# Performance work log

Measured on AMD Instinct MI355X. Metric: run time of the kernel, lower is better.

Reference implementation:

```python
import jax, jax.numpy as jnp
import numpy as np

# Phi-2 config
B, S = 4, 1024            # batch, seq_len (uniform prefill)
T = B * S                 # total tokens
HID = 2560
H = 32                    # attention heads
D = HID // H              # head_size = 80
ROT = int(0.4 * D)        # partial rotary dim = 32
THETA = 10000.0
SCALE = D ** -0.5
NUM_SLOTS = 2 * T


def setup_inputs() -> dict:
    key = jax.random.key(0)
    ks = jax.random.split(key, 6)
    hidden_states = jax.random.normal(ks[0], (T, HID), jnp.float32) * 0.02
    # true rope tables: positions restart per sequence
    pos = jnp.tile(jnp.arange(S, dtype=jnp.float32), B)                 # [T]
    inv_freq = 1.0 / (THETA ** (jnp.arange(0, ROT, 2, dtype=jnp.float32) / ROT))  # [ROT/2]
    freqs = pos[:, None] * inv_freq[None, :]                            # [T, ROT/2]
    cos, sin = jnp.cos(freqs), jnp.sin(freqs)
    slots = jnp.arange(T, dtype=jnp.int32)
    kv_cache_k = jnp.zeros((NUM_SLOTS, H, D), jnp.float32)
    kv_cache_v = jnp.zeros((NUM_SLOTS, H, D), jnp.float32)
    qkv_w = jax.random.normal(ks[1], (3 * HID, HID), jnp.float32) * 0.02
    qkv_b = jax.random.normal(ks[2], (3 * HID,), jnp.float32) * 0.02
    dense_w = jax.random.normal(ks[3], (HID, HID), jnp.float32) * 0.02
    dense_b = jax.random.normal(ks[4], (HID,), jnp.float32) * 0.02
    return {"hidden_states": hidden_states, "cos": cos, "sin": sin, "slots": slots,
            "kv_cache_k": kv_cache_k, "kv_cache_v": kv_cache_v,
            "qkv_w": qkv_w, "qkv_b": qkv_b, "dense_w": dense_w, "dense_b": dense_b}


def _partial_rope(x, cos, sin):
    # x: [T, H, D]; rotate-half rope on the first ROT dims only
    x1 = x[..., : ROT // 2]
    x2 = x[..., ROT // 2 : ROT]
    c = cos[:, None, :]  # [T,1,ROT/2]
    s = sin[:, None, :]
    rot = jnp.concatenate([x1 * c - x2 * s, x1 * s + x2 * c], axis=-1)
    return jnp.concatenate([rot, x[..., ROT:]], axis=-1)


def reference(hidden_states, cos, sin, slots, kv_cache_k, kv_cache_v,
              qkv_w, qkv_b, dense_w, dense_b):
    # fused QKV projection
    qkv = hidden_states @ qkv_w.T + qkv_b                 # [T, 3*HID]
    q = qkv[:, :HID].reshape(T, H, D)
    k = qkv[:, HID:2 * HID].reshape(T, H, D)
    v = qkv[:, 2 * HID:].reshape(T, H, D)
    # partial rotary on q and k
    q = _partial_rope(q, cos, sin)
    k = _partial_rope(k, cos, sin)
    # KV-cache write (reshape_and_cache)
    kc = kv_cache_k.at[slots].set(k)
    vc = kv_cache_v.at[slots].set(v)
    # causal flash-attention (prefill path), uniform seq lengths
    qb = q.reshape(B, S, H, D)
    kb = k.reshape(B, S, H, D)
    vb = v.reshape(B, S, H, D)
    scores = jnp.einsum("bqhd,bkhd->bhqk", qb, kb) * SCALE  # [B,H,S,S]
    causal = jnp.tril(jnp.ones((S, S), bool))
    scores = jnp.where(causal[None, None], scores, jnp.finfo(scores.dtype).min)
    probs = jax.nn.softmax(scores, axis=-1)
    attn = jnp.einsum("bhqk,bkhd->bqhd", probs, vb).reshape(T, HID)
    out = attn @ dense_w.T + dense_b                       # [T, HID]
    return out, kc, vc
```

## Files before the change

### kernel.cpp

```cpp
#include <hip/hip_runtime.h>

#define SEQ    1024
#define NBAT   4
#define TTOK   4096
#define HIDN   2560
#define NQKV   7680
#define NHEAD  32
#define DHEAD  80
#define NSLOT  8192
#define SCALE_F 0.111803398874989485f
#define LOG2E_F 1.4426950408889634f

typedef float  f32x4  __attribute__((ext_vector_type(4)));
typedef __bf16 bf16x8 __attribute__((ext_vector_type(8)));
typedef short  s16x8  __attribute__((ext_vector_type(8)));
typedef short  s16x4  __attribute__((ext_vector_type(4)));
typedef ushort u16x4  __attribute__((ext_vector_type(4)));

typedef __attribute__((address_space(3))) void lds_v;
typedef __attribute__((address_space(1))) void glb_v;

__device__ __forceinline__ void gload16(const void* g, void* l) {
  __builtin_amdgcn_global_load_lds((glb_v*)g, (lds_v*)l, 16, 0, 0);
}

__device__ __forceinline__ f32x4 mfma16(s16x8 a, s16x8 b, f32x4 c) {
  return __builtin_amdgcn_mfma_f32_16x16x32_bf16(
      __builtin_bit_cast(bf16x8, a), __builtin_bit_cast(bf16x8, b), c, 0, 0, 0);
}

__device__ __forceinline__ ushort f2bf(float f) {
  uint u = __builtin_bit_cast(uint, f);
  u += 0x7fffu + ((u >> 16) & 1u);
  return (ushort)(u >> 16);
}
__device__ __forceinline__ float bf2f(ushort h) {
  uint u = (uint)h << 16;
  return __builtin_bit_cast(float, u);
}

#define NQ_HS  2621440
#define NQ_QW  4915200
#define NQ_DW  1638400
#define NQ_PRE (NQ_HS + NQ_QW)
__global__ __launch_bounds__(256)
void prep_kernel(const float* __restrict__ hs, const float* __restrict__ qkvw,
                 ushort* __restrict__ hsb, ushort* __restrict__ qkvwb,
                 uint* __restrict__ flags) {
  const int tid0 = blockIdx.x * 256 + threadIdx.x;
  if (tid0 < NSLOT) flags[tid0] = 0u;
  const int stride = gridDim.x * 256;
  for (int i = tid0; i < NQ_PRE; i += stride) {
    const float* src; ushort* dst; int q;
    if (i < NQ_HS) { src = hs;   dst = hsb;   q = i; }
    else           { src = qkvw; dst = qkvwb; q = i - NQ_HS; }
    float4 v = *(const float4*)(src + q * 4);
    u16x4 o = { f2bf(v.x), f2bf(v.y), f2bf(v.z), f2bf(v.w) };
    *(u16x4*)(dst + q * 4) = o;
  }
}

template<int OUT_BF16>
__global__ __launch_bounds__(512, 2)
void gemm8p(const ushort* __restrict__ A, const ushort* __restrict__ B,
            const float* __restrict__ bias, void* __restrict__ Cout,
            int M, int N, int K, int GX, int RR, int RC) {
  __shared__ ushort sA[3][256 * 64];
  __shared__ ushort sB[2][256 * 64];
  const int tid = threadIdx.x;
  const int l   = tid & 63;
  const int w   = tid >> 6;
  const int wm  = w >> 2, wn = w & 3;
  const int r   = l & 15,  g = l >> 4;

  const int fl  = blockIdx.x;
  const int xcd = fl & 7;
  const int idx = fl >> 3;
  const int cgroups = GX / RC;
  const int rg = xcd / cgroups, cg = xcd % cgroups;
  const int by = rg * RR + idx / RC;
  const int bx = cg * RC + idx % RC;
  const int m0  = by * 256, n0 = bx * 256;
  const int NT  = K >> 6;

  const int srow = w * 16 + (l >> 3);
  const int scol = ((l & 7) ^ (l >> 3)) * 8;
  const ushort* Ab = A + (size_t)(m0 + srow) * K + scol;
  const ushort* Bb = B + (size_t)(n0 + srow) * K + scol;
  const size_t r8   = (size_t)8 * K;
  const size_t r128 = (size_t)128 * K;

#define STG_A(t_, h_, buf_) { \
    const ushort* gp = Ab + (size_t)(t_) * 64 + (size_t)(h_) * r128; \
    char* lp = (char*)(&sA[buf_][0]) + ((h_) * 128 + w * 16) * 128; \
    gload16(gp, lp); gload16(gp + r8, lp + 1024); }
#define STG_B(t_, h_, buf_) { \
    const ushort* gp = Bb + (size_t)(t_) * 64 + (size_t)(h_) * r128; \
    char* lp = (char*)(&sB[buf_][0]) + ((h_) * 128 + w * 16) * 128; \
    gload16(gp, lp); gload16(gp + r8, lp + 1024); }

  const int kswz = (r & 7) * 8;
  const int c0 = (g * 8) ^ kswz;
  const int c1 = (32 + g * 8) ^ kswz;
  const int arow = (wm * 128 + r) * 64;
  const int brow = (wn * 64 + r) * 64;

  f32x4 acc[8][4];
#pragma unroll
  for (int m = 0; m < 8; m++)
#pragma unroll
    for (int n = 0; n < 4; n++) { f32x4 z = {0.f,0.f,0.f,0.f}; acc[m][n] = z; }

  STG_A(0, 0, 0); STG_A(0, 1, 0);
  STG_B(0, 0, 0); STG_B(0, 1, 0);
  STG_A(1, 0, 1); STG_A(1, 1, 1);
  asm volatile("s_waitcnt vmcnt(4)" ::: "memory");
  __builtin_amdgcn_sched_barrier(0);
  __builtin_amdgcn_s_barrier();

#define MFMA_Q(q_) \
    __builtin_amdgcn_s_setprio(1); \
    _Pragma("unroll") \
    for (int n = 0; n < 4; n++) acc[2*(q_)  ][n] = mfma16(x0, b0[n], acc[2*(q_)  ][n]); \
    _Pragma("unroll") \
    for (int n = 0; n < 4; n++) acc[2*(q_)+1][n] = mfma16(y0, b0[n], acc[2*(q_)+1][n]); \
    _Pragma("unroll") \
    for (int n = 0; n < 4; n++) acc[2*(q_)  ][n] = mfma16(x1, b1[n], acc[2*(q_)  ][n]); \
    _Pragma("unroll") \
    for (int n = 0; n < 4; n++) acc[2*(q_)+1][n] = mfma16(y1, b1[n], acc[2*(q_)+1][n]); \
    __builtin_amdgcn_s_setprio(0);

#define LOAD_A(m0_, m1_) \
    x0 = *(const s16x8*)&cA[arow + (m0_) * 1024 + c0]; \
    x1 = *(const s16x8*)&cA[arow + (m0_) * 1024 + c1]; \
    y0 = *(const s16x8*)&cA[arow + (m1_) * 1024 + c0]; \
    y1 = *(const s16x8*)&cA[arow + (m1_) * 1024 + c1];

  int bA = 0;
#pragma unroll 1
  for (int t = 0; t < NT; ++t) {
    const ushort* cA = &sA[bA][0];
    const ushort* cB = &sB[t & 1][0];
    const int nb = (t & 1) ^ 1;
    int a2 = bA + 2; if (a2 >= 3) a2 -= 3;

    s16x8 b0[4], b1[4], x0, x1, y0, y1;

#pragma unroll
    for (int n = 0; n < 4; n++) {
      b0[n] = *(const s16x8*)&cB[brow + n * 1024 + c0];
      b1[n] = *(const s16x8*)&cB[brow + n * 1024 + c1];
    }
    LOAD_A(0, 1)
    if (t + 1 < NT) STG_B(t + 1, 0, nb);
    MFMA_Q(0)

    LOAD_A(2, 3)
    if (t + 1 < NT) STG_B(t + 1, 1, nb);
    MFMA_Q(1)

    LOAD_A(4, 5)
    if (t + 2 < NT) STG_A(t + 2, 0, a2);
    MFMA_Q(2)

    LOAD_A(6, 7)
    if (t + 2 < NT) STG_A(t + 2, 1, a2);
    MFMA_Q(3)
    if (t < NT - 2) {
      asm volatile("s_waitcnt vmcnt(4)" ::: "memory");
    } else if (t == NT - 2) {
      asm volatile("s_waitcnt vmcnt(0)" ::: "memory");
    }
    __builtin_amdgcn_sched_barrier(0);
    __builtin_amdgcn_s_barrier();

    bA++; if (bA >= 3) bA = 0;
  }

#pragma unroll
  for (int n = 0; n < 4; n++) {
    const int col = n0 + wn * 64 + n * 16 + r;
    const float bv = bias[col];
#pragma unroll
    for (int m = 0; m < 8; m++) {
      const int row = m0 + wm * 128 + m * 16 + g * 4;
#pragma unroll
      for (int j = 0; j < 4; j++) {
        float v = acc[m][n][j] + bv;
        if (OUT_BF16) ((ushort*)Cout)[(size_t)(row + j) * N + col] = f2bf(v);
        else          ((float*)Cout)[(size_t)(row + j) * N + col] = v;
      }
    }
  }
#undef STG_A
#undef STG_B
#undef MFMA_Q
#undef LOAD_A
}

template<int OUT_BF16>
__global__ __launch_bounds__(256)
void gemm_nt(const ushort* __restrict__ A, const ushort* __restrict__ B,
             const float* __restrict__ bias, void* __restrict__ Cout,
             int M, int N, int K, int GX, int RR, int RC) {
  __shared__ ushort lsA[128 * 32];
  __shared__ ushort lsB[128 * 32];
  const int tid  = threadIdx.x;
  const int lane = tid & 63;
  const int w    = tid >> 6;
  const int wr   = w >> 1, wc = w & 1;
  const int r    = lane & 15, g = lane >> 4;

  const int fl  = blockIdx.x;
  const int xcd = fl & 7;
  const int idx = fl >> 3;
  const int cgroups = GX / RC;
  const int rg = xcd / cgroups, cg = xcd % cgroups;
  const int by = rg * RR + idx / RC;
  const int bx = cg * RC + idx % RC;
  const int m0 = by * 128, n0 = bx * 128;

  const int row0 = tid >> 2;
  const int kc0  = (tid & 3) * 8;

  f32x4 acc[4][4];
#pragma unroll
  for (int i = 0; i < 4; i++)
#pragma unroll
    for (int j = 0; j < 4; j++) { f32x4 z = {0.f,0.f,0.f,0.f}; acc[i][j] = z; }

  const ushort* Abase = A + (size_t)m0 * K;
  const ushort* Bbase = B + (size_t)n0 * K;
  char* dstA0 = (char*)lsA + (size_t)(w * 64) * 16;
  char* dstA1 = (char*)lsA + (size_t)(256 + w * 64) * 16;
  char* dstB0 = (char*)lsB + (size_t)(w * 64) * 16;
  char* dstB1 = (char*)lsB + (size_t)(256 + w * 64) * 16;

  for (int k0 = 0; k0 < K; k0 += 32) {
    gload16(Abase + (size_t)row0 * K + k0 + kc0,        dstA0);
    gload16(Abase + (size_t)(64 + row0) * K + k0 + kc0, dstA1);
    gload16(Bbase + (size_t)row0 * K + k0 + kc0,        dstB0);
    gload16(Bbase + (size_t)(64 + row0) * K + k0 + kc0, dstB1);
    __syncthreads();

    s16x8 af[4], bfr[4];
#pragma unroll
    for (int f = 0; f < 4; f++) {
      af[f]  = *(const s16x8*)&lsA[(wr * 64 + f * 16 + r) * 32 + g * 8];
      bfr[f] = *(const s16x8*)&lsB[(wc * 64 + f * 16 + r) * 32 + g * 8];
    }
#pragma unroll
    for (int fi = 0; fi < 4; fi++)
#pragma unroll
      for (int fj = 0; fj < 4; fj++)
        acc[fi][fj] = mfma16(af[fi], bfr[fj], acc[fi][fj]);
    __syncthreads();
  }

#pragma unroll
  for (int fj = 0; fj < 4; fj++) {
    const int col = n0 + wc * 64 + fj * 16 + r;
    const float bv = bias[col];
#pragma unroll
    for (int fi = 0; fi < 4; fi++) {
      const int row = m0 + wr * 64 + fi * 16 + g * 4;
#pragma unroll
      for (int j = 0; j < 4; j++) {
        float v = acc[fi][fj][j] + bv;
        if (OUT_BF16) ((ushort*)Cout)[(size_t)(row + j) * N + col] = f2bf(v);
        else          ((float*)Cout)[(size_t)(row + j) * N + col] = v;
      }
    }
  }
}

__global__ __launch_bounds__(256)
void rope_scatter(ushort* __restrict__ qkv, const float* __restrict__ cosp,
                  const float* __restrict__ sinp, const int* __restrict__ slots,
                  float* __restrict__ kc, float* __restrict__ vc,
                  uint* __restrict__ flags) {
  const int t = blockIdx.x;
  const int tid = threadIdx.x;
  __shared__ float cs[16], sn[16];
  if (tid < 16)       cs[tid]      = cosp[t * 16 + tid];
  else if (tid < 32)  sn[tid - 16] = sinp[t * 16 + tid - 16];
  __syncthreads();
  const int slot = slots[t];
  if (tid == 0) flags[slot] = 1u;
  ushort* qrow = qkv + (size_t)t * NQKV;
  float* kcr = kc + (size_t)slot * HIDN;
  float* vcr = vc + (size_t)slot * HIDN;

  for (int idx = tid; idx < 512; idx += 256) {
    int hh = idx >> 4, i = idx & 15;
    ushort* p = qrow + hh * DHEAD + i;
    float x1 = bf2f(p[0]), x2 = bf2f(p[16]);
    float c = cs[i], s = sn[i];
    p[0]  = f2bf(x1 * c - x2 * s);
    p[16] = f2bf(x1 * s + x2 * c);
  }
  for (int idx = tid; idx < 512; idx += 256) {
    int hh = idx >> 4, i = idx & 15;
    ushort* p = qrow + HIDN + hh * DHEAD + i;
    float x1 = bf2f(p[0]), x2 = bf2f(p[16]);
    float c = cs[i], s = sn[i];
    float k1 = x1 * c - x2 * s, k2 = x1 * s + x2 * c;
    p[0]  = f2bf(k1);
    p[16] = f2bf(k2);
    kcr[hh * DHEAD + i]      = k1;
    kcr[hh * DHEAD + i + 16] = k2;
  }
  for (int idx = tid; idx < 1536; idx += 256) {
    int hh = idx / 48, d = 32 + idx % 48;
    kcr[hh * DHEAD + d] = bf2f(qrow[HIDN + hh * DHEAD + d]);
  }
  for (int idx = tid; idx < HIDN; idx += 256) {
    vcr[idx] = bf2f(qrow[2 * HIDN + idx]);
  }
}

__global__ __launch_bounds__(512, 4)
void mega_kernel(const ushort* __restrict__ qkv, ushort* __restrict__ attn_out,
                 const float* __restrict__ kin, const float* __restrict__ vin,
                 const uint* __restrict__ flags,
                 float* __restrict__ kout, float* __restrict__ vout,
                 const float* __restrict__ densew, ushort* __restrict__ densewb) {
  __shared__ ushort lsK[64 * 104];
  __shared__ ushort lsVT[80 * 68];
  __shared__ ushort lsP[8][16 * 68];
  const int bid = blockIdx.x;

  if (bid >= 1024) {
    if (bid < 5120) {
      const int row = (bid - 1024) * 2 + (threadIdx.x >> 8);
      const int t2  = threadIdx.x & 255;
      if (flags[row]) return;
      const float4* ks = (const float4*)(kin + (size_t)row * HIDN);
      const float4* vs = (const float4*)(vin + (size_t)row * HIDN);
      float4* kd = (float4*)(kout + (size_t)row * HIDN);
      float4* vd = (float4*)(vout + (size_t)row * HIDN);
      for (int i = t2; i < HIDN / 4; i += 256) { kd[i] = ks[i]; vd[i] = vs[i]; }
    } else {
      int i = (bid - 5120) * 512 + threadIdx.x;
      for (; i < NQ_DW; i += 256 * 512) {
        float4 v = *(const float4*)(densew + i * 4);
        u16x4 o = { f2bf(v.x), f2bf(v.y), f2bf(v.z), f2bf(v.w) };
        *(u16x4*)(densewb + i * 4) = o;
      }
    }
    return;
  }

  const int qb = 7 - (bid >> 7);
  const int hb = bid & 127;
  const int h = hb & 31, b = hb >> 5;
  const int tid  = threadIdx.x;
  const int lane = tid & 63, w = tid >> 6;
  const int r    = lane & 15, g = lane >> 4;

  {
    int kv = tid >> 3, cp = tid & 7;
    *(uint*)&lsK[kv * 104 + 80 + cp * 2] = 0u;
  }

  const size_t qrow = (size_t)(b * SEQ + qb * 128 + w * 16 + r);
  const ushort* qp = qkv + qrow * NQKV + h * DHEAD;
  s16x8 qf[3];
  qf[0] = *(const s16x8*)(qp + g * 8);
  qf[1] = *(const s16x8*)(qp + 32 + g * 8);
  if (g < 2) qf[2] = *(const s16x8*)(qp + 64 + g * 8);
  else { s16x8 z = {0,0,0,0,0,0,0,0}; qf[2] = z; }

  int off_g[5]; uint off_kv[5];
#pragma unroll
  for (int j = 0; j < 5; j++) {
    int i = tid + j * 512;
    int kv = i / 40, dp = i - kv * 40;
    off_g[j]  = kv * NQKV + dp * 2;
    off_kv[j] = (uint)(kv * 104 + dp * 2) | ((uint)(dp * 2 * 68 + kv) << 16);
  }
  const ushort* kvbase = qkv + (size_t)(b * SEQ) * NQKV + HIDN + h * DHEAD;

  uint kreg[5], vreg[5];
#pragma unroll
  for (int j = 0; j < 5; j++) {
    kreg[j] = *(const uint*)(kvbase + off_g[j]);
    vreg[j] = *(const uint*)(kvbase + off_g[j] + HIDN);
  }

  float m_run[4] = {-1e30f, -1e30f, -1e30f, -1e30f};
  float l_run[4] = {0.f, 0.f, 0.f, 0.f};
  f32x4 acco[5];
#pragma unroll
  for (int nb = 0; nb < 5; nb++) { f32x4 z = {0.f,0.f,0.f,0.f}; acco[nb] = z; }

  const int ntiles = 2 * qb + 2;
  for (int t = 0; t < ntiles; t++) {
#pragma unroll
    for (int j = 0; j < 5; j++) {
      int ok = off_kv[j] & 0xffff, ov = off_kv[j] >> 16;
      *(uint*)&lsK[ok] = kreg[j];
      uint vv = vreg[j];
      lsVT[ov]      = (ushort)(vv & 0xffffu);
      lsVT[ov + 68] = (ushort)(vv >> 16);
    }
    __syncthreads();

    if (t + 1 < ntiles) {
      const ushort* nb_ = kvbase + (size_t)(t + 1) * 64 * NQKV;
#pragma unroll
      for (int j = 0; j < 5; j++) {
        kreg[j] = *(const uint*)(nb_ + off_g[j]);
        vreg[j] = *(const uint*)(nb_ + off_g[j] + HIDN);
      }
    }

    f32x4 sacc[4];
#pragma unroll
    for (int cb = 0; cb < 4; cb++) {
      f32x4 acc = {0.f, 0.f, 0.f, 0.f};
#pragma unroll
      for (int c = 0; c < 3; c++) {
        s16x8 kf = *(const s16x8*)&lsK[(cb * 16 + r) * 104 + c * 32 + g * 8];
        acc = mfma16(qf[c], kf, acc);
      }
      sacc[cb] = acc;
    }

    const bool diag = (t >= 2 * qb);
    const int kv0 = t * 64;
    const int q0  = qb * 128 + w * 16 + g * 4;
#pragma unroll
    for (int cb = 0; cb < 4; cb++)
#pragma unroll
      for (int j = 0; j < 4; j++) {
        float s = sacc[cb][j] * SCALE_F;
        if (diag && (kv0 + cb * 16 + r) > (q0 + j)) s = -1e30f;
        sacc[cb][j] = s;
      }

    float mnew[4], alpha[4], rs[4];
#pragma unroll
    for (int j = 0; j < 4; j++) {
      float m = fmaxf(fmaxf(sacc[0][j], sacc[1][j]), fmaxf(sacc[2][j], sacc[3][j]));
      m = fmaxf(m, __shfl_xor(m, 1));
      m = fmaxf(m, __shfl_xor(m, 2));
      m = fmaxf(m, __shfl_xor(m, 4));
      m = fmaxf(m, __shfl_xor(m, 8));
      mnew[j]  = fmaxf(m_run[j], m);
      alpha[j] = exp2f((m_run[j] - mnew[j]) * LOG2E_F);
      m_run[j] = mnew[j];
      rs[j] = 0.f;
    }

#pragma unroll
    for (int cb = 0; cb < 4; cb++)
#pragma unroll
      for (int j = 0; j < 4; j++) {
        float p = exp2f((sacc[cb][j] - mnew[j]) * LOG2E_F);
        rs[j] += p;
        lsP[w][(g * 4 + j) * 68 + cb * 16 + r] = f2bf(p);
      }

#pragma unroll
    for (int j = 0; j < 4; j++) {
      float v = rs[j];
      v += __shfl_xor(v, 1);
      v += __shfl_xor(v, 2);
      v += __shfl_xor(v, 4);
      v += __shfl_xor(v, 8);
      l_run[j] = l_run[j] * alpha[j] + v;
#pragma unroll
      for (int nb = 0; nb < 5; nb++) acco[nb][j] *= alpha[j];
    }

    s16x8 pa[2];
#pragma unroll
    for (int ch = 0; ch < 2; ch++) {
      s16x4 lo = *(const s16x4*)&lsP[w][r * 68 + ch * 32 + g * 8];
      s16x4 hi = *(const s16x4*)&lsP[w][r * 68 + ch * 32 + g * 8 + 4];
      pa[ch] = __builtin_shufflevector(lo, hi, 0, 1, 2, 3, 4, 5, 6, 7);
    }

#pragma unroll
    for (int nb = 0; nb < 5; nb++)
#pragma unroll
      for (int ch = 0; ch < 2; ch++) {
        s16x4 lo = *(const s16x4*)&lsVT[(nb * 16 + r) * 68 + ch * 32 + g * 8];
        s16x4 hi = *(const s16x4*)&lsVT[(nb * 16 + r) * 68 + ch * 32 + g * 8 + 4];
        s16x8 vf = __builtin_shufflevector(lo, hi, 0, 1, 2, 3, 4, 5, 6, 7);
        acco[nb] = mfma16(pa[ch], vf, acco[nb]);
      }

    __syncthreads();
  }

  const size_t orow = (size_t)(b * SEQ + qb * 128 + w * 16 + g * 4);
#pragma unroll
  for (int j = 0; j < 4; j++) {
    float inv = 1.0f / l_run[j];
#pragma unroll
    for (int nb = 0; nb < 5; nb++)
      attn_out[(orow + j) * HIDN + h * DHEAD + nb * 16 + r] = f2bf(acco[nb][j] * inv);
  }
}

extern "C" void kernel_launch(void* const* d_in, const int* in_sizes, int n_in,
                              void* d_out, int out_size, void* d_ws, size_t ws_size,
                              hipStream_t stream) {
  (void)in_sizes; (void)n_in; (void)out_size; (void)ws_size;
  const float* hs      = (const float*)d_in[0];
  const float* cosp    = (const float*)d_in[1];
  const float* sinp    = (const float*)d_in[2];
  const int*   slots   = (const int*)  d_in[3];
  const float* kck_in  = (const float*)d_in[4];
  const float* kcv_in  = (const float*)d_in[5];
  const float* qkvw    = (const float*)d_in[6];
  const float* qkvb    = (const float*)d_in[7];
  const float* densew  = (const float*)d_in[8];
  const float* denseb  = (const float*)d_in[9];

  float* out    = (float*)d_out;
  float* kc_out = out + (size_t)TTOK * HIDN;
  float* vc_out = kc_out + (size_t)NSLOT * HIDN;

  char* ws = (char*)d_ws;
  ushort* hsb     = (ushort*)(ws);
  ushort* attnb   = (ushort*)(ws);
  ushort* qkvwb   = (ushort*)(ws + 20971520);
  ushort* densewb = (ushort*)(ws + 60293120);
  ushort* qkvb16  = (ushort*)(ws + 73400320);
  uint*   flags   = (uint*)(ws + 136314880);

  prep_kernel<<<2048, 256, 0, stream>>>(hs, qkvw, hsb, qkvwb, flags);

  gemm8p<1><<<480, 512, 0, stream>>>(hsb, qkvwb, qkvb, qkvb16, TTOK, NQKV, HIDN, 30, 4, 15);

  rope_scatter<<<TTOK, 256, 0, stream>>>(qkvb16, cosp, sinp, slots, kc_out, vc_out, flags);

  mega_kernel<<<5376, 512, 0, stream>>>(qkvb16, attnb, kck_in, kcv_in, flags,
                                        kc_out, vc_out, densew, densewb);

  gemm_nt<0><<<640, 256, 0, stream>>>(
      attnb, densewb, denseb, out, TTOK, HIDN, HIDN, 20, 8, 10);
}
```

Baseline: 415.9 us.

## Double-buffer dense GEMM with swizzled BK=64 LDS tiles and attention K/V tiles

Replaces the dense output GEMM with a double-buffered version that uses 64-wide K tiles. The LDS layout is XOR-swizzled and the next tile is prefetched while the current one feeds the MFMAs. The change also adds setprio around the MFMA block and uses launch bounds of 256 threads with a minimum of 2 blocks. In the attention kernel, K and V^T LDS tiles are double-buffered so the trailing barrier per iteration can be dropped, at the cost of twice the LDS for those tiles (about 48KB per block versus about 31KB before), which may lower occupancy.

```diff
diff --git a/kernel.cpp b/kernel.cpp
--- a/kernel.cpp
+++ b/kernel.cpp
@@ -198,18 +198,17 @@
 #undef LOAD_A
 }
 
-template<int OUT_BF16>
-__global__ __launch_bounds__(256)
-void gemm_nt(const ushort* __restrict__ A, const ushort* __restrict__ B,
-             const float* __restrict__ bias, void* __restrict__ Cout,
+__global__ __launch_bounds__(256, 2)
+void gemm_db(const ushort* __restrict__ A, const ushort* __restrict__ B,
+             const float* __restrict__ bias, float* __restrict__ Cout,
              int M, int N, int K, int GX, int RR, int RC) {
-  __shared__ ushort lsA[128 * 32];
-  __shared__ ushort lsB[128 * 32];
-  const int tid  = threadIdx.x;
-  const int lane = tid & 63;
-  const int w    = tid >> 6;
-  const int wr   = w >> 1, wc = w & 1;
-  const int r    = lane & 15, g = lane >> 4;
+  __shared__ ushort sA[2][128 * 64];
+  __shared__ ushort sB[2][128 * 64];
+  const int tid = threadIdx.x;
+  const int l   = tid & 63;
+  const int w   = tid >> 6;
+  const int wm  = w >> 1, wn = w & 1;
+  const int r   = l & 15,  g = l >> 4;
 
   const int fl  = blockIdx.x;
   const int xcd = fl & 7;
@@ -219,59 +218,98 @@
   const int by = rg * RR + idx / RC;
   const int bx = cg * RC + idx % RC;
   const int m0 = by * 128, n0 = bx * 128;
-
-  const int row0 = tid >> 2;
-  const int kc0  = (tid & 3) * 8;
+  const int NT = K >> 6;
+
+  const int srow = w * 16 + (l >> 3);
+  const int scol = ((l & 7) ^ (l >> 3)) * 8;
+  const ushort* Ab = A + (size_t)(m0 + srow) * K + scol;
+  const ushort* Bb = B + (size_t)(n0 + srow) * K + scol;
+  const size_t r8  = (size_t)8 * K;
+  const size_t r64 = (size_t)64 * K;
+
+#define DSTG_A(t_, h_, buf_) { \
+    const ushort* gp = Ab + (size_t)(t_) * 64 + (size_t)(h_) * r64; \
+    char* lp = (char*)(&sA[buf_][0]) + ((h_) * 64 + w * 16) * 128; \
+    gload16(gp, lp); gload16(gp + r8, lp + 1024); }
+#define DSTG_B(t_, h_, buf_) { \
+    const ushort* gp = Bb + (size_t)(t_) * 64 + (size_t)(h_) * r64; \
+    char* lp = (char*)(&sB[buf_][0]) + ((h_) * 64 + w * 16) * 128; \
+    gload16(gp, lp); gload16(gp + r8, lp + 1024); }
+
+  const int kswz = (r & 7) * 8;
+  const int c0 = (g * 8) ^ kswz;
+  const int c1 = (32 + g * 8) ^ kswz;
+  const int arow = (wm * 64 + r) * 64;
+  const int brow = (wn * 64 + r) * 64;
 
   f32x4 acc[4][4];
 #pragma unroll
-  for (int i = 0; i < 4; i++)
-#pragma unroll
-    for (int j = 0; j < 4; j++) { f32x4 z = {0.f,0.f,0.f,0.f}; acc[i][j] = z; }
-
-  const ushort* Abase = A + (size_t)m0 * K;
-  const ushort* Bbase = B + (size_t)n0 * K;
-  char* dstA0 = (char*)lsA + (size_t)(w * 64) * 16;
-  char* dstA1 = (char*)lsA + (size_t)(256 + w * 64) * 16;
-  char* dstB0 = (char*)lsB + (size_t)(w * 64) * 16;
-  char* dstB1 = (char*)lsB + (size_t)(256 + w * 64) * 16;
-
-  for (int k0 = 0; k0 < K; k0 += 32) {
-    gload16(Abase + (size_t)row0 * K + k0 + kc0,        dstA0);
-    gload16(Abase + (size_t)(64 + row0) * K + k0 + kc0, dstA1);
-    gload16(Bbase + (size_t)row0 * K + k0 + kc0,        dstB0);
-    gload16(Bbase + (size_t)(64 + row0) * K + k0 + kc0, dstB1);
-    __syncthreads();
-
-    s16x8 af[4], bfr[4];
-#pragma unroll
-    for (int f = 0; f < 4; f++) {
-      af[f]  = *(const s16x8*)&lsA[(wr * 64 + f * 16 + r) * 32 + g * 8];
-      bfr[f] = *(const s16x8*)&lsB[(wc * 64 + f * 16 + r) * 32 + g * 8];
-    }
-#pragma unroll
-    for (int fi = 0; fi < 4; fi++)
-#pragma unroll
-      for (int fj = 0; fj < 4; fj++)
-        acc[fi][fj] = mfma16(af[fi], bfr[fj], acc[fi][fj]);
-    __syncthreads();
-  }
-
-#pragma unroll
-  for (int fj = 0; fj < 4; fj++) {
-    const int col = n0 + wc * 64 + fj * 16 + r;
-    const float bv = bias[col];
-#pragma unroll
-    for (int fi = 0; fi < 4; fi++) {
-      const int row = m0 + wr * 64 + fi * 16 + g * 4;
-#pragma unroll
-      for (int j = 0; j < 4; j++) {
-        float v = acc[fi][fj][j] + bv;
-        if (OUT_BF16) ((ushort*)Cout)[(size_t)(row + j) * N + col] = f2bf(v);
-        else          ((float*)Cout)[(size_t)(row + j) * N + col] = v;
-      }
-    }
-  }
+  for (int m = 0; m < 4; m++)
+#pragma unroll
+    for (int n = 0; n < 4; n++) { f32x4 z = {0.f,0.f,0.f,0.f}; acc[m][n] = z; }
+
+  DSTG_A(0, 0, 0); DSTG_A(0, 1, 0);
+  DSTG_B(0, 0, 0); DSTG_B(0, 1, 0);
+  asm volatile("s_waitcnt vmcnt(0)" ::: "memory");
+  __builtin_amdgcn_sched_barrier(0);
+  __builtin_amdgcn_s_barrier();
+
+#pragma unroll 1
+  for (int t = 0; t < NT; ++t) {
+    const int cur = t & 1, nxt = cur ^ 1;
+    const ushort* cA = &sA[cur][0];
+    const ushort* cB = &sB[cur][0];
+
+    if (t + 1 < NT) {
+      DSTG_A(t + 1, 0, nxt); DSTG_A(t + 1, 1, nxt);
+      DSTG_B(t + 1, 0, nxt); DSTG_B(t + 1, 1, nxt);
+    }
+
+    s16x8 av[4], aw[4], bv[4], bw[4];
+#pragma unroll
+    for (int n = 0; n < 4; n++) {
+      bv[n] = *(const s16x8*)&cB[brow + n * 1024 + c0];
+      bw[n] = *(const s16x8*)&cB[brow + n * 1024 + c1];
+    }
+#pragma unroll
+    for (int m = 0; m < 4; m++) {
+      av[m] = *(const s16x8*)&cA[arow + m * 1024 + c0];
+      aw[m] = *(const s16x8*)&cA[arow + m * 1024 + c1];
+    }
+    __builtin_amdgcn_s_setprio(1);
+#pragma unroll
+    for (int m = 0; m < 4; m++)
+#pragma unroll
+      for (int n = 0; n < 4; n++)
+        acc[m][n] = mfma16(av[m], bv[n], acc[m][n]);
+#pragma unroll
+    for (int m = 0; m < 4; m++)
+#pragma unroll
+      for (int n = 0; n < 4; n++)
+        acc[m][n] = mfma16(aw[m], bw[n], acc[m][n]);
+    __builtin_amdgcn_s_setprio(0);
+
+    if (t + 1 < NT) {
+      asm volatile("s_waitcnt vmcnt(0)" ::: "memory");
+      __builtin_amdgcn_sched_barrier(0);
+      __builtin_amdgcn_s_barrier();
+    }
+  }
+
+#pragma unroll
+  for (int n = 0; n < 4; n++) {
+    const int col = n0 + wn * 64 + n * 16 + r;
+    const float bv2 = bias[col];
+#pragma unroll
+    for (int m = 0; m < 4; m++) {
+      const int row = m0 + wm * 64 + m * 16 + g * 4;
+#pragma unroll
+      for (int j = 0; j < 4; j++)
+        Cout[(size_t)(row + j) * N + col] = acc[m][n][j] + bv2;
+    }
+  }
+#undef DSTG_A
+#undef DSTG_B
 }
 
 __global__ __launch_bounds__(256)
@@ -325,8 +363,8 @@
                  const uint* __restrict__ flags,
                  float* __restrict__ kout, float* __restrict__ vout,
                  const float* __restrict__ densew, ushort* __restrict__ densewb) {
-  __shared__ ushort lsK[64 * 104];
-  __shared__ ushort lsVT[80 * 68];
+  __shared__ ushort lsK[2][64 * 104];
+  __shared__ ushort lsVT[2][80 * 68];
   __shared__ ushort lsP[8][16 * 68];
   const int bid = blockIdx.x;
 
@@ -360,7 +398,8 @@
 
   {
     int kv = tid >> 3, cp = tid & 7;
-    *(uint*)&lsK[kv * 104 + 80 + cp * 2] = 0u;
+    *(uint*)&lsK[0][kv * 104 + 80 + cp * 2] = 0u;
+    *(uint*)&lsK[1][kv * 104 + 80 + cp * 2] = 0u;
   }
 
   const size_t qrow = (size_t)(b * SEQ + qb * 128 + w * 16 + r);
@@ -396,13 +435,16 @@
 
   const int ntiles = 2 * qb + 2;
   for (int t = 0; t < ntiles; t++) {
+    const int cur = t & 1;
+    ushort* curK  = &lsK[cur][0];
+    ushort* curVT = &lsVT[cur][0];
 #pragma unroll
     for (int j = 0; j < 5; j++) {
       int ok = off_kv[j] & 0xffff, ov = off_kv[j] >> 16;
-      *(uint*)&lsK[ok] = kreg[j];
+      *(uint*)&curK[ok] = kreg[j];
       uint vv = vreg[j];
-      lsVT[ov]      = (ushort)(vv & 0xffffu);
-      lsVT[ov + 68] = (ushort)(vv >> 16);
+      curVT[ov]      = (ushort)(vv & 0xffffu);
+      curVT[ov + 68] = (ushort)(vv >> 16);
     }
     __syncthreads();
 
@@ -421,7 +463,7 @@
       f32x4 acc = {0.f, 0.f, 0.f, 0.f};
 #pragma unroll
       for (int c = 0; c < 3; c++) {
-        s16x8 kf = *(const s16x8*)&lsK[(cb * 16 + r) * 104 + c * 32 + g * 8];
+        s16x8 kf = *(const s16x8*)&curK[(cb * 16 + r) * 104 + c * 32 + g * 8];
         acc = mfma16(qf[c], kf, acc);
       }
       sacc[cb] = acc;
@@ -486,13 +528,11 @@
     for (int nb = 0; nb < 5; nb++)
 #pragma unroll
       for (int ch = 0; ch < 2; ch++) {
-        s16x4 lo = *(const s16x4*)&lsVT[(nb * 16 + r) * 68 + ch * 32 + g * 8];
-        s16x4 hi = *(const s16x4*)&lsVT[(nb * 16 + r) * 68 + ch * 32 + g * 8 + 4];
+        s16x4 lo = *(const s16x4*)&curVT[(nb * 16 + r) * 68 + ch * 32 + g * 8];
+        s16x4 hi = *(const s16x4*)&curVT[(nb * 16 + r) * 68 + ch * 32 + g * 8 + 4];
         s16x8 vf = __builtin_shufflevector(lo, hi, 0, 1, 2, 3, 4, 5, 6, 7);
         acco[nb] = mfma16(pa[ch], vf, acco[nb]);
       }
-
-    __syncthreads();
   }
 
   const size_t orow = (size_t)(b * SEQ + qb * 128 + w * 16 + g * 4);
@@ -541,6 +581,6 @@
   mega_kernel<<<5376, 512, 0, stream>>>(qkvb16, attnb, kck_in, kcv_in, flags,
                                         kc_out, vc_out, densew, densewb);
 
-  gemm_nt<0><<<640, 256, 0, stream>>>(
+  gemm_db<<<640, 256, 0, stream>>>(
       attnb, densewb, denseb, out, TTOK, HIDN, HIDN, 20, 8, 10);
 }
```

Result: no change. 423.8 us (+1.9%).
